# Optimization experiments

Hardware: AMD Instinct MI355X
Metric: run time of the kernel (lower is better)

Reference implementation:

```python
import jax, jax.numpy as jnp
import numpy as np

N = 100000   # num nodes
E = 1600000  # num edges
D = 128      # input_dim == hidden_dim == output_dim
EPS_BN = 1e-5
EPS_LN = 1e-5


def setup_inputs() -> dict:
    key = jax.random.key(0)
    ks = jax.random.split(key, 20)
    s = 0.05
    x = jax.random.normal(ks[0], (N, D), jnp.float32)
    edge_index = jax.random.randint(ks[1], (2, E), 0, N, dtype=jnp.int64)
    p = lambda k, shape: jax.random.normal(k, shape, jnp.float32) * s
    return {
        "x": x,
        "edge_index": edge_index,
        # GCNConv layers: weight stored [in, out], bias [out]
        "W0": p(ks[2], (D, D)), "b0": jnp.zeros((D,), jnp.float32),
        "W1": p(ks[3], (D, D)), "b1": jnp.zeros((D,), jnp.float32),
        "W2": p(ks[4], (D, D)), "b2": jnp.zeros((D,), jnp.float32),
        # BatchNorm affine params
        "g0": jnp.ones((D,), jnp.float32), "be0": jnp.zeros((D,), jnp.float32),
        "g1": jnp.ones((D,), jnp.float32), "be1": jnp.zeros((D,), jnp.float32),
        # MHA: seq_len=1 -> only v and out projections affect output
        "Wv": p(ks[5], (D, D)), "bv": jnp.zeros((D,), jnp.float32),
        "Wo": p(ks[6], (D, D)), "bo": jnp.zeros((D,), jnp.float32),
        # attention LayerNorm
        "ln_g": jnp.ones((D,), jnp.float32), "ln_b": jnp.zeros((D,), jnp.float32),
    }


def gcn_conv(x, W, b, row, col, n):
    """PyG GCNConv: h = D^-1/2 (A+I) D^-1/2 (x W) + b, symmetric norm with self-loops."""
    h = x @ W  # [N, out]
    deg = jax.ops.segment_sum(jnp.ones((row.shape[0],), h.dtype), col, num_segments=n) + 1.0
    dinv = jax.lax.rsqrt(deg)                                   # [N]
    msg = h[row] * (dinv[row] * dinv[col])[:, None]              # [E, out] gather
    agg = jax.ops.segment_sum(msg, col, num_segments=n)          # [N, out] scatter-add
    return agg + h * (dinv * dinv)[:, None] + b                  # self-loop term + bias


def batch_norm(x, g, b):
    mu = x.mean(0)
    var = x.var(0)
    return (x - mu) * jax.lax.rsqrt(var + EPS_BN) * g + b


def layer_norm(x, g, b):
    mu = x.mean(-1, keepdims=True)
    var = x.var(-1, keepdims=True)
    return (x - mu) * jax.lax.rsqrt(var + EPS_LN) * g + b


def reference(x, edge_index, W0, b0, W1, b1, W2, b2, g0, be0, g1, be1,
              Wv, bv, Wo, bo, ln_g, ln_b):
    row, col = edge_index[0], edge_index[1]
    # layer 0: conv -> BN -> relu -> (+residual; input_dim==hidden so identity residual)
    res = x
    h = gcn_conv(x, W0, b0, row, col, N)
    h = jax.nn.relu(batch_norm(h, g0, be0)) + res
    # middle layer (i=1)
    res = h
    h = gcn_conv(h, W1, b1, row, col, N)
    h = jax.nn.relu(batch_norm(h, g1, be1)) + res
    # MHA over seq_len=1: softmax over a single key is 1, so out = out_proj(v_proj(h))
    att = (h @ Wv + bv) @ Wo + bo
    h = layer_norm(h + att, ln_g, ln_b)
    # output conv
    return gcn_conv(h, W2, b2, row, col, N)
```

## Files before the change

kernel.cpp:

```cpp
#include <hip/hip_runtime.h>
#include <hip/hip_bf16.h>

#define N_NODES 100000
#define N_EDGES 1600000
#define DD 128
#define EPS_BN 1e-5f
#define EPS_LN 1e-5f
#define CAP 48
#define GRP_NODES 12500
#define FILL_GRP 256
#define BIN_BLOCKS 512
#define NTH (BIN_BLOCKS * 256)
#define BCAP 1024
#define GSTRIDE (BIN_BLOCKS * BCAP)

typedef __attribute__((ext_vector_type(4))) float floatx4;
typedef __attribute__((ext_vector_type(8))) short short8;
typedef __attribute__((ext_vector_type(4))) short short4v;
typedef __attribute__((ext_vector_type(2))) unsigned uint2v;

__device__ inline unsigned short f2bf(float f) {
  unsigned u = __builtin_bit_cast(unsigned, f);
  unsigned r = (u + 0x7FFFu + ((u >> 16) & 1u)) >> 16;
  return (unsigned short)r;
}
__device__ inline float bf2f(unsigned short s) {
  unsigned u = ((unsigned)s) << 16;
  return __builtin_bit_cast(float, u);
}
__device__ inline float bflo(unsigned u) { return __builtin_bit_cast(float, u << 16); }
__device__ inline float bfhi(unsigned u) {
  return __builtin_bit_cast(float, u & 0xFFFF0000u);
}

__global__ __launch_bounds__(1024) void detect_kernel(const int* __restrict__ ei,
                                                      int* __restrict__ flag) {
  __shared__ int nz;
  if (threadIdx.x == 0) nz = 0;
  __syncthreads();
  int v = ei[threadIdx.x * 2 + 1];
  if (v != 0) atomicAdd(&nz, 1);
  __syncthreads();
  if (threadIdx.x == 0) flag[0] = (nz == 0) ? 1 : 0;
}

__global__ void init_kernel(int* __restrict__ cnt, float* __restrict__ sums) {
  int i = blockIdx.x * blockDim.x + threadIdx.x;
  if (i < N_NODES) cnt[i] = 0;
  if (i < 512) sums[i] = 0.f;
}

template <int K>
__device__ inline void place_rec(const int* r, const int* c, const int* gid, int lane,
                                 unsigned long long below,
                                 unsigned (*stage)[BCAP], int* lcnt) {
  unsigned pk[K];
#pragma unroll
  for (int k = 0; k < K; ++k) {
    int g = gid[k] >= 0 ? gid[k] : 0;
    pk[k] = ((unsigned)r[k] << 14) | (unsigned)(c[k] - g * GRP_NODES);
  }
#pragma unroll
  for (int g = 0; g < 8; ++g) {
    unsigned long long m[K];
    int off[K];
    int tot = 0;
#pragma unroll
    for (int k = 0; k < K; ++k) {
      m[k] = __ballot(gid[k] == g);
      off[k] = tot;
      tot += __popcll(m[k]);
    }
    if (tot == 0) continue;
    int base = 0;
    if (lane == 0) base = atomicAdd(&lcnt[g], tot);
    base = __shfl(base, 0);
#pragma unroll
    for (int k = 0; k < K; ++k) {
      if (gid[k] == g) {
        int pos = base + off[k] + __popcll(m[k] & below);
        if (pos < BCAP) stage[g][pos] = pk[k];
      }
    }
  }
}

__global__ __launch_bounds__(256) void bin_stage_kernel(const int* __restrict__ ei,
                                                        const int* __restrict__ flag,
                                                        unsigned* __restrict__ binned,
                                                        int* __restrict__ bcnt) {
  __shared__ unsigned stage[8][BCAP];
  __shared__ int lcnt[8];
  const int tid = threadIdx.x;
  if (tid < 8) lcnt[tid] = 0;
  __syncthreads();

  const int t = blockIdx.x * 256 + tid;
  const int lane = tid & 63;
  const unsigned long long below = (1ull << lane) - 1ull;
  const int f = flag[0];

  if (f) {
#pragma unroll
    for (int it = 0; it < 7; ++it) {
      int p = t + it * NTH;
      bool v = p < (N_EDGES / 2);
      int4 rv = make_int4(0, 0, 0, 0), cv = make_int4(0, 0, 0, 0);
      if (v) {
        rv = *(const int4*)(ei + 4 * p);
        cv = *(const int4*)(ei + 2 * N_EDGES + 4 * p);
      }
      int r[2] = {rv.x, rv.z};
      int c[2] = {cv.x, cv.z};
      int gid[2] = {v ? cv.x / GRP_NODES : -1, v ? cv.z / GRP_NODES : -1};
      place_rec<2>(r, c, gid, lane, below, stage, lcnt);
    }
  } else {
#pragma unroll
    for (int it = 0; it < 4; ++it) {
      int q = t + it * NTH;
      bool v = q < (N_EDGES / 4);
      int4 rv = make_int4(0, 0, 0, 0), cv = make_int4(0, 0, 0, 0);
      if (v) {
        rv = *(const int4*)(ei + 4 * q);
        cv = *(const int4*)(ei + N_EDGES + 4 * q);
      }
      int r[4] = {rv.x, rv.y, rv.z, rv.w};
      int c[4] = {cv.x, cv.y, cv.z, cv.w};
      int gid[4] = {v ? cv.x / GRP_NODES : -1, v ? cv.y / GRP_NODES : -1,
                    v ? cv.z / GRP_NODES : -1, v ? cv.w / GRP_NODES : -1};
      place_rec<4>(r, c, gid, lane, below, stage, lcnt);
    }
  }
  __syncthreads();

  const int b = blockIdx.x;
#pragma unroll
  for (int g = 0; g < 8; ++g) {
    int n = lcnt[g] < BCAP ? lcnt[g] : BCAP;
    for (int i = tid; i < n; i += 256) {
      binned[g * GSTRIDE + b * BCAP + i] = stage[g][i];
    }
  }
  if (tid < 8) {
    int n = lcnt[tid] < BCAP ? lcnt[tid] : BCAP;
    bcnt[b * 8 + tid] = n;
  }
}

__global__ __launch_bounds__(256) void fill_group_kernel(const unsigned* __restrict__ binned,
                                                         const int* __restrict__ bcnt,
                                                         int* __restrict__ cnt,
                                                         unsigned* __restrict__ epos) {
  const int g = blockIdx.x & 7;
  const int bg = blockIdx.x >> 3;
  const int lo = g * GRP_NODES;
  for (int i = bg * 256 + threadIdx.x; i < GSTRIDE; i += FILL_GRP * 256) {
    int b = i >> 10;
    int slot = i & (BCAP - 1);
    if (slot < bcnt[b * 8 + g]) {
      unsigned pk = binned[g * GSTRIDE + i];
      int c = lo + (int)(pk & 16383u);
      int r = (int)(pk >> 14);
      int p = atomicAdd(&cnt[c], 1);
      if (p < CAP) epos[c * CAP + p] = (unsigned)r;
    }
  }
}

__global__ void prep_w_kernel(const float* __restrict__ W0, const float* __restrict__ W1,
                              const float* __restrict__ W2, unsigned short* __restrict__ Wt) {
  int id = blockIdx.x * blockDim.x + threadIdx.x;
  if (id >= 3 * DD * DD) return;
  int mat = id / (DD * DD);
  int rem = id % (DD * DD);
  int k = rem / DD;
  int n = rem % DD;
  const float* W = (mat == 0) ? W0 : (mat == 1) ? W1 : W2;
  Wt[mat * DD * DD + n * DD + k] = f2bf(W[k * DD + n]);
}

__global__ void prep_mha_kernel(const float* __restrict__ Wv, const float* __restrict__ Wo,
                                const float* __restrict__ bv, const float* __restrict__ bo,
                                unsigned short* __restrict__ Wt5, float* __restrict__ biasp) {
  int id = blockIdx.x * blockDim.x + threadIdx.x;
  if (id < DD * DD) {
    int k = id >> 7, n = id & 127;
    float acc = 0.f;
    for (int j = 0; j < DD; ++j) acc += Wv[k * DD + j] * Wo[j * DD + n];
    Wt5[n * DD + k] = f2bf(acc);
  } else if (id < DD * DD + DD) {
    int n = id - DD * DD;
    float acc = bo[n];
    for (int j = 0; j < DD; ++j) acc += bv[j] * Wo[j * DD + n];
    biasp[n] = acc;
  }
}

template <typename AT>
__global__ __launch_bounds__(256) void gemm_bf16_kernel(const AT* __restrict__ A,
                                                        const unsigned short* __restrict__ Wt,
                                                        const int* __restrict__ cnt,
                                                        unsigned short* __restrict__ C) {
  __shared__ short Ws[128][136];
  const int tid = threadIdx.x;
  const int rowbase = blockIdx.x * 128;

#pragma unroll
  for (int i = 0; i < 8; ++i) {
    int ch = tid + i * 256;
    int r = ch >> 4;
    int c = (ch & 15) << 3;
    *(int4*)(&Ws[r][c]) = *(const int4*)(Wt + r * DD + c);
  }

  const int lane = tid & 63;
  const int wv = tid >> 6;
  const int m = lane & 15;
  const int q = lane >> 4;
  const int r0 = wv * 32;

  int row0 = rowbase + r0 + m;
  int row1 = rowbase + r0 + 16 + m;
  if (row0 >= N_NODES) row0 = N_NODES - 1;
  if (row1 >= N_NODES) row1 = N_NODES - 1;
  short8 a0[4], a1[4];
  if constexpr (__is_same(AT, float)) {
    const float* A0 = A + row0 * DD;
    const float* A1 = A + row1 * DD;
#pragma unroll
    for (int kc = 0; kc < 4; ++kc) {
      float4 v0 = *(const float4*)(A0 + kc * 32 + q * 8);
      float4 v1 = *(const float4*)(A0 + kc * 32 + q * 8 + 4);
      float4 w0 = *(const float4*)(A1 + kc * 32 + q * 8);
      float4 w1 = *(const float4*)(A1 + kc * 32 + q * 8 + 4);
      short8 s0, s1;
      s0[0] = (short)f2bf(v0.x); s0[1] = (short)f2bf(v0.y);
      s0[2] = (short)f2bf(v0.z); s0[3] = (short)f2bf(v0.w);
      s0[4] = (short)f2bf(v1.x); s0[5] = (short)f2bf(v1.y);
      s0[6] = (short)f2bf(v1.z); s0[7] = (short)f2bf(v1.w);
      s1[0] = (short)f2bf(w0.x); s1[1] = (short)f2bf(w0.y);
      s1[2] = (short)f2bf(w0.z); s1[3] = (short)f2bf(w0.w);
      s1[4] = (short)f2bf(w1.x); s1[5] = (short)f2bf(w1.y);
      s1[6] = (short)f2bf(w1.z); s1[7] = (short)f2bf(w1.w);
      a0[kc] = s0;
      a1[kc] = s1;
    }
  } else {
    const unsigned short* A0 = A + row0 * DD;
    const unsigned short* A1 = A + row1 * DD;
#pragma unroll
    for (int kc = 0; kc < 4; ++kc) {
      a0[kc] = *(const short8*)(A0 + kc * 32 + q * 8);
      a1[kc] = *(const short8*)(A1 + kc * 32 + q * 8);
    }
  }
  __syncthreads();

  floatx4 acc[2][8];
#pragma unroll
  for (int t = 0; t < 2; ++t)
#pragma unroll
    for (int n = 0; n < 8; ++n) acc[t][n] = (floatx4){0.f, 0.f, 0.f, 0.f};

#pragma unroll
  for (int kc = 0; kc < 4; ++kc) {
    int k = kc * 32 + q * 8;
#pragma unroll
    for (int n = 0; n < 8; ++n) {
      short8 b = *(const short8*)(&Ws[n * 16 + m][k]);
      acc[0][n] = __builtin_amdgcn_mfma_f32_16x16x32_bf16(a0[kc], b, acc[0][n], 0, 0, 0);
      acc[1][n] = __builtin_amdgcn_mfma_f32_16x16x32_bf16(a1[kc], b, acc[1][n], 0, 0, 0);
    }
  }

  __syncthreads();
#pragma unroll
  for (int t = 0; t < 2; ++t) {
#pragma unroll
    for (int r = 0; r < 4; ++r) {
      int rl = r0 + t * 16 + q * 4 + r;
      int row = rowbase + rl;
      float sc = (row < N_NODES) ? rsqrtf((float)cnt[row] + 1.0f) : 0.f;
#pragma unroll
      for (int n = 0; n < 8; ++n) {
        Ws[rl][n * 16 + m] = (short)f2bf(acc[t][n][r] * sc);
      }
    }
  }
  __syncthreads();
#pragma unroll
  for (int i = 0; i < 8; ++i) {
    int ch = tid + i * 256;
    int r = ch >> 4;
    int c = (ch & 15) << 3;
    int row = rowbase + r;
    if (row < N_NODES) *(int4*)(C + row * DD + c) = *(const int4*)(&Ws[r][c]);
  }
}

__global__ __launch_bounds__(256) void gemm_mha_ln_kernel(
    const unsigned short* __restrict__ A, const unsigned short* __restrict__ Wt,
    const float* __restrict__ biasp, const float* __restrict__ lng,
    const float* __restrict__ lnb, unsigned short* __restrict__ C) {
  __shared__ short As[128][136];
  __shared__ short Ws[128][136];
  const int tid = threadIdx.x;
  const int rowbase = blockIdx.x * 128;

#pragma unroll
  for (int i = 0; i < 8; ++i) {
    int ch = tid + i * 256;
    int r = ch >> 4;
    int c = (ch & 15) << 3;
    *(int4*)(&Ws[r][c]) = *(const int4*)(Wt + r * DD + c);
  }
#pragma unroll
  for (int i = 0; i < 8; ++i) {
    int ch = tid + i * 256;
    int r = ch >> 4;
    int c = (ch & 15) << 3;
    int row = rowbase + r;
    int4 v = make_int4(0, 0, 0, 0);
    if (row < N_NODES) v = *(const int4*)(A + row * DD + c);
    *(int4*)(&As[r][c]) = v;
  }
  __syncthreads();

  const int lane = tid & 63;
  const int wv = tid >> 6;
  const int m = lane & 15;
  const int q = lane >> 4;
  const int r0 = wv * 32;

  floatx4 acc[2][8];
#pragma unroll
  for (int t = 0; t < 2; ++t)
#pragma unroll
    for (int n = 0; n < 8; ++n) acc[t][n] = (floatx4){0.f, 0.f, 0.f, 0.f};

#pragma unroll
  for (int kc = 0; kc < 4; ++kc) {
    int k = kc * 32 + q * 8;
    short8 a0 = *(const short8*)(&As[r0 + m][k]);
    short8 a1 = *(const short8*)(&As[r0 + 16 + m][k]);
#pragma unroll
    for (int n = 0; n < 8; ++n) {
      short8 b = *(const short8*)(&Ws[n * 16 + m][k]);
      acc[0][n] = __builtin_amdgcn_mfma_f32_16x16x32_bf16(a0, b, acc[0][n], 0, 0, 0);
      acc[1][n] = __builtin_amdgcn_mfma_f32_16x16x32_bf16(a1, b, acc[1][n], 0, 0, 0);
    }
  }
  __syncthreads();

  float bp[8], gg[8], bb[8];
#pragma unroll
  for (int n = 0; n < 8; ++n) {
    int col = n * 16 + m;
    bp[n] = biasp[col];
    gg[n] = lng[col];
    bb[n] = lnb[col];
  }

#pragma unroll
  for (int t = 0; t < 2; ++t) {
#pragma unroll
    for (int r = 0; r < 4; ++r) {
      int rl = r0 + t * 16 + q * 4 + r;
      float v[8];
      float s = 0.f, ss = 0.f;
#pragma unroll
      for (int n = 0; n < 8; ++n) {
        float val = acc[t][n][r] + bp[n] + bf2f((unsigned short)As[rl][n * 16 + m]);
        v[n] = val;
        s += val;
        ss += val * val;
      }
#pragma unroll
      for (int o = 1; o <= 8; o <<= 1) {
        s += __shfl_xor(s, o, 64);
        ss += __shfl_xor(ss, o, 64);
      }
      float mu = s * (1.f / 128.f);
      float var = ss * (1.f / 128.f) - mu * mu;
      float rs = rsqrtf(var + EPS_LN);
#pragma unroll
      for (int n = 0; n < 8; ++n) {
        Ws[rl][n * 16 + m] = (short)f2bf((v[n] - mu) * rs * gg[n] + bb[n]);
      }
    }
  }
  __syncthreads();
#pragma unroll
  for (int i = 0; i < 8; ++i) {
    int ch = tid + i * 256;
    int r = ch >> 4;
    int c = (ch & 15) << 3;
    int row = rowbase + r;
    if (row < N_NODES) *(int4*)(C + row * DD + c) = *(const int4*)(&Ws[r][c]);
  }
}

template <typename OT>
__global__ __launch_bounds__(256) void aggregate_kernel(const uint2v* __restrict__ hw2,
                                                        const unsigned* __restrict__ epos,
                                                        const int* __restrict__ cnt,
                                                        const float* __restrict__ bias,
                                                        OT* __restrict__ out) {
  int node = (blockIdx.x * blockDim.x + threadIdx.x) >> 6;
  int lane = threadIdx.x & 63;
  if (node >= N_NODES) return;
  node = __builtin_amdgcn_readfirstlane(node);
  const int half = lane >> 5;
  const int lc = lane & 31;
  int deg = cnt[node];
  int s = node * CAP;
  int e = s + (deg < CAP ? deg : CAP);
  float a0 = 0.f, a1 = 0.f, a2 = 0.f, a3 = 0.f;
  for (int p = s; p < e; p += 16) {
    int idx[8];
    float msk[8];
    uint2v u[8];
#pragma unroll
    for (int j = 0; j < 8; ++j) {
      int i = p + 2 * j + half;
      idx[j] = (int)epos[(i < e) ? i : (e - 1)];
      msk[j] = (i < e) ? 1.f : 0.f;
    }
#pragma unroll
    for (int j = 0; j < 8; ++j) u[j] = hw2[idx[j] * 32 + lc];
#pragma unroll
    for (int j = 0; j < 8; ++j) {
      a0 += msk[j] * bflo(u[j].x);
      a1 += msk[j] * bfhi(u[j].x);
      a2 += msk[j] * bflo(u[j].y);
      a3 += msk[j] * bfhi(u[j].y);
    }
  }
  a0 += __shfl_xor(a0, 32, 64);
  a1 += __shfl_xor(a1, 32, 64);
  a2 += __shfl_xor(a2, 32, 64);
  a3 += __shfl_xor(a3, 32, 64);
  uint2v uh = hw2[node * 32 + lc];
  float dv = rsqrtf((float)deg + 1.0f);
  float4 b = ((const float4*)bias)[lc];
  float o0 = (a0 + bflo(uh.x)) * dv + b.x;
  float o1 = (a1 + bfhi(uh.x)) * dv + b.y;
  float o2 = (a2 + bflo(uh.y)) * dv + b.z;
  float o3 = (a3 + bfhi(uh.y)) * dv + b.w;
  if (half == 0) {
    if constexpr (__is_same(OT, float)) {
      float4 o = make_float4(o0, o1, o2, o3);
      ((float4*)out)[node * 32 + lc] = o;
    } else {
      uint2v o;
      o.x = (unsigned)f2bf(o0) | ((unsigned)f2bf(o1) << 16);
      o.y = (unsigned)f2bf(o2) | ((unsigned)f2bf(o3) << 16);
      ((uint2v*)out)[node * 32 + lc] = o;
    }
  }
}

__global__ void bn_stats_kernel(const unsigned short* __restrict__ in,
                                float* __restrict__ sum, float* __restrict__ sumsq) {
  int col = threadIdx.x;
  float s = 0.f, ss = 0.f;
  for (int r = blockIdx.x; r < N_NODES; r += gridDim.x) {
    float v = bf2f(in[r * DD + col]);
    s += v;
    ss += v * v;
  }
  atomicAdd(&sum[col], s);
  atomicAdd(&sumsq[col], ss);
}

template <typename RT>
__global__ void bn_norm_kernel(const unsigned short* __restrict__ in,
                               const float* __restrict__ sum, const float* __restrict__ sumsq,
                               const float* __restrict__ g, const float* __restrict__ be,
                               const RT* __restrict__ res, unsigned short* __restrict__ out) {
  int idx = blockIdx.x * blockDim.x + threadIdx.x;
  if (idx >= N_NODES * 32) return;
  int c4 = (idx & 31) << 2;
  short4v v = ((const short4v*)in)[idx];
  float r4[4];
  if constexpr (__is_same(RT, float)) {
    float4 r = ((const float4*)res)[idx];
    r4[0] = r.x; r4[1] = r.y; r4[2] = r.z; r4[3] = r.w;
  } else {
    short4v r = ((const short4v*)res)[idx];
    r4[0] = bf2f((unsigned short)r.x);
    r4[1] = bf2f((unsigned short)r.y);
    r4[2] = bf2f((unsigned short)r.z);
    r4[3] = bf2f((unsigned short)r.w);
  }
  const float invn = 1.0f / (float)N_NODES;
  short4v o;
#pragma unroll
  for (int j = 0; j < 4; ++j) {
    int c = c4 + j;
    float mu = sum[c] * invn;
    float var = sumsq[c] * invn - mu * mu;
    float sc = g[c] * rsqrtf(var + EPS_BN);
    float x = bf2f((unsigned short)((const short*)&v)[j]);
    float y = (x - mu) * sc + be[c];
    y = fmaxf(y, 0.f) + r4[j];
    ((short*)&o)[j] = (short)f2bf(y);
  }
  ((short4v*)out)[idx] = o;
}

extern "C" void kernel_launch(void* const* d_in, const int* in_sizes, int n_in,
                              void* d_out, int out_size, void* d_ws, size_t ws_size,
                              hipStream_t stream) {
  const float* x = (const float*)d_in[0];
  const int* ei = (const int*)d_in[1];
  const float* W0 = (const float*)d_in[2];
  const float* b0 = (const float*)d_in[3];
  const float* W1 = (const float*)d_in[4];
  const float* b1 = (const float*)d_in[5];
  const float* W2 = (const float*)d_in[6];
  const float* b2 = (const float*)d_in[7];
  const float* g0 = (const float*)d_in[8];
  const float* be0 = (const float*)d_in[9];
  const float* g1 = (const float*)d_in[10];
  const float* be1 = (const float*)d_in[11];
  const float* Wv = (const float*)d_in[12];
  const float* bv = (const float*)d_in[13];
  const float* Wo = (const float*)d_in[14];
  const float* bo = (const float*)d_in[15];
  const float* lng = (const float*)d_in[16];
  const float* lnb = (const float*)d_in[17];
  float* outp = (float*)d_out;

  char* w = (char*)d_ws;
  unsigned short* Gb = (unsigned short*)(w + 0);
  unsigned short* h1b = (unsigned short*)(w + 25600000);
  unsigned short* h2b = (unsigned short*)(w + 51200000);
  unsigned* epos = (unsigned*)(w + 76800000);
  int* cnt = (int*)(w + 96000000);
  float* sums = (float*)(w + 96400256);
  unsigned short* Wt = (unsigned short*)(w + 96402816);
  unsigned short* Wt5 = Wt + 3 * DD * DD;
  float* biasp = (float*)(w + 96533888);
  int* flag = (int*)(w + 96534400);
  unsigned* binned = (unsigned*)Gb;
  int* bcnt = (int*)(w + 16777216);
  unsigned short* aggB = (unsigned short*)d_out;

  detect_kernel<<<1, 1024, 0, stream>>>(ei, flag);
  init_kernel<<<(N_NODES + 255) / 256, 256, 0, stream>>>(cnt, sums);
  bin_stage_kernel<<<BIN_BLOCKS, 256, 0, stream>>>(ei, flag, binned, bcnt);
  fill_group_kernel<<<8 * FILL_GRP, 256, 0, stream>>>(binned, bcnt, cnt, epos);
  prep_w_kernel<<<(3 * DD * DD + 255) / 256, 256, 0, stream>>>(W0, W1, W2, Wt);
  prep_mha_kernel<<<(DD * DD + DD + 255) / 256, 256, 0, stream>>>(Wv, Wo, bv, bo, Wt5, biasp);

  const int GB = (N_NODES + 127) / 128;
  const int AB = (N_NODES + 3) / 4;
  const int EB = (N_NODES * 32 + 255) / 256;

  gemm_bf16_kernel<float><<<GB, 256, 0, stream>>>(x, Wt + 0 * DD * DD, cnt, Gb);
  aggregate_kernel<unsigned short><<<AB, 256, 0, stream>>>((const uint2v*)Gb, epos, cnt, b0,
                                                           aggB);
  bn_stats_kernel<<<512, 128, 0, stream>>>(aggB, sums + 0, sums + 128);
  bn_norm_kernel<float><<<EB, 256, 0, stream>>>(aggB, sums + 0, sums + 128, g0, be0, x, h1b);

  gemm_bf16_kernel<unsigned short><<<GB, 256, 0, stream>>>(h1b, Wt + 1 * DD * DD, cnt, Gb);
  aggregate_kernel<unsigned short><<<AB, 256, 0, stream>>>((const uint2v*)Gb, epos, cnt, b1,
                                                           aggB);
  bn_stats_kernel<<<512, 128, 0, stream>>>(aggB, sums + 256, sums + 384);
  bn_norm_kernel<unsigned short><<<EB, 256, 0, stream>>>(aggB, sums + 256, sums + 384, g1, be1,
                                                         h1b, h2b);

  gemm_mha_ln_kernel<<<GB, 256, 0, stream>>>(h2b, Wt5, biasp, lng, lnb, h1b);

  gemm_bf16_kernel<unsigned short><<<GB, 256, 0, stream>>>(h1b, Wt + 2 * DD * DD, cnt, Gb);
  aggregate_kernel<float><<<AB, 256, 0, stream>>>((const uint2v*)Gb, epos, cnt, b2, outp);
}
```

Baseline: 623.6 us.

## Build padded CSR per node sub-range in shared memory instead of global atomics

Replaces the global-atomic fill kernel with a CSR build kernel. Each block owns a 391-node sub-range of a group, scans every binned edge of that group, and accumulates neighbor slots with shared-memory atomics before writing counts and padded edge lists to global memory coalesced. This removes the cnt zeroing and the scattered global atomics, but each block now rereads the whole group's binned data (32x redundant reads), and only 256 blocks run. BCAP also drops from 1024 to 640 per bin block, which could overflow and silently drop edges if a bin exceeds 640 entries.

```diff
diff --git a/kernel.cpp b/kernel.cpp
--- a/kernel.cpp
+++ b/kernel.cpp
@@ -8,11 +8,12 @@
 #define EPS_LN 1e-5f
 #define CAP 48
 #define GRP_NODES 12500
-#define FILL_GRP 256
 #define BIN_BLOCKS 512
 #define NTH (BIN_BLOCKS * 256)
-#define BCAP 1024
+#define BCAP 640
 #define GSTRIDE (BIN_BLOCKS * BCAP)
+#define SUBN 391
+#define NSB 32
 
 typedef __attribute__((ext_vector_type(4))) float floatx4;
 typedef __attribute__((ext_vector_type(8))) short short8;
@@ -44,9 +45,8 @@
   if (threadIdx.x == 0) flag[0] = (nz == 0) ? 1 : 0;
 }
 
-__global__ void init_kernel(int* __restrict__ cnt, float* __restrict__ sums) {
+__global__ void init_kernel(float* __restrict__ sums) {
   int i = blockIdx.x * blockDim.x + threadIdx.x;
-  if (i < N_NODES) cnt[i] = 0;
   if (i < 512) sums[i] = 0.f;
 }
 
@@ -148,24 +148,43 @@
   }
 }
 
-__global__ __launch_bounds__(256) void fill_group_kernel(const unsigned* __restrict__ binned,
-                                                         const int* __restrict__ bcnt,
-                                                         int* __restrict__ cnt,
-                                                         unsigned* __restrict__ epos) {
+__global__ __launch_bounds__(256) void csr_build_kernel(const unsigned* __restrict__ binned,
+                                                        const int* __restrict__ bcnt,
+                                                        int* __restrict__ cnt,
+                                                        unsigned* __restrict__ epos) {
+  __shared__ unsigned slots[SUBN][CAP];
+  __shared__ int hist[SUBN];
+  __shared__ int lbcnt[BIN_BLOCKS];
+  const int tid = threadIdx.x;
   const int g = blockIdx.x & 7;
-  const int bg = blockIdx.x >> 3;
-  const int lo = g * GRP_NODES;
-  for (int i = bg * 256 + threadIdx.x; i < GSTRIDE; i += FILL_GRP * 256) {
-    int b = i >> 10;
-    int slot = i & (BCAP - 1);
-    if (slot < bcnt[b * 8 + g]) {
-      unsigned pk = binned[g * GSTRIDE + i];
-      int c = lo + (int)(pk & 16383u);
-      int r = (int)(pk >> 14);
-      int p = atomicAdd(&cnt[c], 1);
-      if (p < CAP) epos[c * CAP + p] = (unsigned)r;
-    }
-  }
+  const int sb = blockIdx.x >> 3;
+  const int lo_local = sb * SUBN;
+  const int nn = (GRP_NODES - lo_local) < SUBN ? (GRP_NODES - lo_local) : SUBN;
+
+  for (int k = tid; k < SUBN; k += 256) hist[k] = 0;
+  for (int b = tid; b < BIN_BLOCKS; b += 256) lbcnt[b] = bcnt[b * 8 + g];
+  __syncthreads();
+
+  const unsigned* G = binned + (size_t)g * GSTRIDE;
+  for (int b = 0; b < BIN_BLOCKS; ++b) {
+    int n = lbcnt[b];
+    const unsigned* S = G + b * BCAP;
+    for (int i = tid; i < n; i += 256) {
+      unsigned pk = S[i];
+      int cl = (int)(pk & 16383u) - lo_local;
+      if ((unsigned)cl < (unsigned)nn) {
+        int pos = atomicAdd(&hist[cl], 1);
+        if (pos < CAP) slots[cl][pos] = pk >> 14;
+      }
+    }
+  }
+  __syncthreads();
+
+  const int nbase = g * GRP_NODES + lo_local;
+  for (int k = tid; k < nn; k += 256) cnt[nbase + k] = hist[k];
+  unsigned* E = epos + (size_t)nbase * CAP;
+  const unsigned* SL = &slots[0][0];
+  for (int idx = tid; idx < nn * CAP; idx += 256) E[idx] = SL[idx];
 }
 
 __global__ void prep_w_kernel(const float* __restrict__ W0, const float* __restrict__ W1,
@@ -549,9 +568,9 @@
   unsigned short* aggB = (unsigned short*)d_out;
 
   detect_kernel<<<1, 1024, 0, stream>>>(ei, flag);
-  init_kernel<<<(N_NODES + 255) / 256, 256, 0, stream>>>(cnt, sums);
+  init_kernel<<<2, 256, 0, stream>>>(sums);
   bin_stage_kernel<<<BIN_BLOCKS, 256, 0, stream>>>(ei, flag, binned, bcnt);
-  fill_group_kernel<<<8 * FILL_GRP, 256, 0, stream>>>(binned, bcnt, cnt, epos);
+  csr_build_kernel<<<8 * NSB, 256, 0, stream>>>(binned, bcnt, cnt, epos);
   prep_w_kernel<<<(3 * DD * DD + 255) / 256, 256, 0, stream>>>(W0, W1, W2, Wt);
   prep_mha_kernel<<<(DD * DD + DD + 255) / 256, 256, 0, stream>>>(Wv, Wo, bv, bo, Wt5, biasp);
 
```

After: 890.4 us. +42.8%, slower.
